# Kernel tuning notes

Hardware: AMD Instinct MI355X
Metric: run time of the kernel (lower is better)

## Reference

```python
import jax, jax.numpy as jnp
import numpy as np


def setup_inputs() -> dict:
    key = jax.random.key(0)
    ks = jax.random.split(key, 7)
    B, IN, H = 4096, 2048, 2048
    initrange = 1.0 / np.sqrt(H)
    return {
        "x": jax.random.normal(ks[0], (B, IN), dtype=jnp.float32),
        "h_prev": jax.random.normal(ks[1], (B, H), dtype=jnp.float32),
        "c_prev": jax.random.normal(ks[2], (B, H), dtype=jnp.float32),
        "W_x": jax.random.uniform(ks[3], (4 * H, IN), minval=-initrange, maxval=initrange, dtype=jnp.float32),
        "b_x": jax.random.uniform(ks[4], (4 * H,), minval=-initrange, maxval=initrange, dtype=jnp.float32),
        "W_h": jax.random.uniform(ks[5], (4 * H, H), minval=-initrange, maxval=initrange, dtype=jnp.float32),
        "b_h": jax.random.uniform(ks[6], (4 * H,), minval=-initrange, maxval=initrange, dtype=jnp.float32),
    }


def reference(x, h_prev, c_prev, W_x, b_x, W_h, b_h):
    # gates = Linear_x(x) + Linear_h(h_prev), shape [B, 4H]
    gates = x @ W_x.T + b_x + h_prev @ W_h.T + b_h
    i, f, g, o = jnp.split(gates, 4, axis=1)  # chunk order in original: i, f, g, o
    i = jax.nn.sigmoid(i)
    f = jax.nn.sigmoid(f)
    g = jnp.tanh(g)
    o = jax.nn.sigmoid(o)
    c = f * c_prev + i * g
    h = o * jnp.tanh(c)
    return (h, c)
```

## Files before the change

### kernel.cpp

```cpp
#include <hip/hip_runtime.h>
#include <hip/hip_bf16.h>
#include <stdint.h>


#define M_DIM 4096
#define N_PACK 8192
#define K_DIM 4096
#define H_DIM 2048

typedef __attribute__((ext_vector_type(8))) short bf16x8;
typedef __attribute__((ext_vector_type(4))) float f32x4;
typedef __attribute__((ext_vector_type(8))) unsigned short ushortx8;

__device__ __forceinline__ unsigned short f2bf(float f) {
    union { float f; uint32_t u; } v; v.f = f;
    uint32_t u = v.u;
    uint32_t r = (u + 0x7FFFu + ((u >> 16) & 1u)) >> 16;
    return (unsigned short)r;
}

__device__ __forceinline__ float fsigmoid(float x) { return 1.0f / (1.0f + __expf(-x)); }
__device__ __forceinline__ float ftanh(float x) { return 2.0f * fsigmoid(2.0f * x) - 1.0f; }

__global__ __launch_bounds__(256) void pack_a(const float* __restrict__ x,
                                              const float* __restrict__ h,
                                              unsigned short* __restrict__ A) {
    int i = blockIdx.x * 256 + threadIdx.x;
    int e = i * 8;
    int row = e >> 12;
    int col = e & 4095;
    const float* src = (col < H_DIM) ? (x + (size_t)row * H_DIM + col)
                                     : (h + (size_t)row * H_DIM + (col - H_DIM));
    float4 f0 = ((const float4*)src)[0];
    float4 f1 = ((const float4*)src)[1];
    ushortx8 o;
    o[0] = f2bf(f0.x); o[1] = f2bf(f0.y); o[2] = f2bf(f0.z); o[3] = f2bf(f0.w);
    o[4] = f2bf(f1.x); o[5] = f2bf(f1.y); o[6] = f2bf(f1.z); o[7] = f2bf(f1.w);
    *(ushortx8*)(A + e) = o;
}

__global__ __launch_bounds__(256) void pack_w(const float* __restrict__ Wx,
                                              const float* __restrict__ Wh,
                                              unsigned short* __restrict__ W) {
    int i = blockIdx.x * 256 + threadIdx.x;
    int e = i * 8;
    int p = e >> 12;
    int k = e & 4095;
    int g  = (p >> 4) & 3;
    int j  = ((p >> 6) << 4) | (p & 15);
    int orig = g * H_DIM + j;
    const float* src = (k < H_DIM) ? (Wx + (size_t)orig * H_DIM + k)
                                   : (Wh + (size_t)orig * H_DIM + (k - H_DIM));
    float4 f0 = ((const float4*)src)[0];
    float4 f1 = ((const float4*)src)[1];
    ushortx8 o;
    o[0] = f2bf(f0.x); o[1] = f2bf(f0.y); o[2] = f2bf(f0.z); o[3] = f2bf(f0.w);
    o[4] = f2bf(f1.x); o[5] = f2bf(f1.y); o[6] = f2bf(f1.z); o[7] = f2bf(f1.w);
    *(ushortx8*)(W + (size_t)p * K_DIM + k) = o;
}

__device__ __forceinline__ void gload_lds16(const void* g, void* l) {
    __builtin_amdgcn_global_load_lds(
        (const __attribute__((address_space(1))) void*)g,
        (__attribute__((address_space(3))) void*)l, 16, 0, 0);
}

__global__ __launch_bounds__(256, 2) void lstm_gemm(
        const unsigned short* __restrict__ A,
        const unsigned short* __restrict__ W,
        const float* __restrict__ bx, const float* __restrict__ bh,
        const float* __restrict__ c_prev, float* __restrict__ out) {
    __shared__ unsigned short Asm[128 * 64];
    __shared__ unsigned short Bsm[128 * 64];

    const int tid  = threadIdx.x;
    const int wid  = tid >> 6;
    const int lane = tid & 63;
    const int bid  = blockIdx.x;
    const int bm   = bid & 31;
    const int bn   = bid >> 5;
    const int wr   = wid >> 1;
    const int wc   = wid & 1;

    f32x4 acc[4][4] = {};

    const char* Abase = (const char*)A + (size_t)(bm * 128) * (K_DIM * 2);
    const char* Wbase = (const char*)W + (size_t)(bn * 128) * (K_DIM * 2);

    int srow[4], skbs[4];
    #pragma unroll
    for (int q = 0; q < 4; ++q) {
        int chunk = wid * 4 + q;
        int o = chunk * 1024 + lane * 16;
        int row = o >> 7;
        int kb  = o & 127;
        srow[q] = row;
        skbs[q] = kb ^ ((row & 7) << 4);
    }

    for (int kt = 0; kt < K_DIM / 64; ++kt) {
        #pragma unroll
        for (int q = 0; q < 4; ++q) {
            int chunk = wid * 4 + q;
            const char* ga = Abase + (size_t)srow[q] * (K_DIM * 2) + kt * 128 + skbs[q];
            const char* gb = Wbase + (size_t)srow[q] * (K_DIM * 2) + kt * 128 + skbs[q];
            gload_lds16(ga, (char*)Asm + chunk * 1024);
            gload_lds16(gb, (char*)Bsm + chunk * 1024);
        }
        __syncthreads();

        #pragma unroll
        for (int kk = 0; kk < 2; ++kk) {
            bf16x8 af[4], bfr[4];
            #pragma unroll
            for (int m = 0; m < 4; ++m) {
                int row = wr * 64 + m * 16 + (lane & 15);
                int cb  = (kk * 64 + ((lane >> 4) << 4)) ^ ((row & 7) << 4);
                af[m] = *(const bf16x8*)((const char*)Asm + row * 128 + cb);
            }
            #pragma unroll
            for (int n = 0; n < 4; ++n) {
                int row = wc * 64 + n * 16 + (lane & 15);
                int cb  = (kk * 64 + ((lane >> 4) << 4)) ^ ((row & 7) << 4);
                bfr[n] = *(const bf16x8*)((const char*)Bsm + row * 128 + cb);
            }
            #pragma unroll
            for (int m = 0; m < 4; ++m)
                #pragma unroll
                for (int n = 0; n < 4; ++n)
                    acc[m][n] = __builtin_amdgcn_mfma_f32_16x16x32_bf16(
                        af[m], bfr[n], acc[m][n], 0, 0, 0);
        }
        __syncthreads();
    }

    const int jlo  = lane & 15;
    const int rgrp = lane >> 4;
    const int pb   = bn * 128 + wc * 64;
    const int j    = ((pb >> 6) << 4) + jlo;

    const float bi  = bx[j]             + bh[j];
    const float bff = bx[H_DIM + j]     + bh[H_DIM + j];
    const float bg  = bx[2 * H_DIM + j] + bh[2 * H_DIM + j];
    const float bo  = bx[3 * H_DIM + j] + bh[3 * H_DIM + j];

    float* out_h = out;
    float* out_c = out + (size_t)M_DIM * H_DIM;

    #pragma unroll
    for (int m = 0; m < 4; ++m) {
        int row0 = bm * 128 + wr * 64 + m * 16 + rgrp * 4;
        #pragma unroll
        for (int r = 0; r < 4; ++r) {
            int row = row0 + r;
            float pi = acc[m][0][r] + bi;
            float pf = acc[m][1][r] + bff;
            float pg = acc[m][2][r] + bg;
            float po = acc[m][3][r] + bo;
            float i_ = fsigmoid(pi);
            float f_ = fsigmoid(pf);
            float g_ = ftanh(pg);
            float o_ = fsigmoid(po);
            float cp = c_prev[(size_t)row * H_DIM + j];
            float c  = f_ * cp + i_ * g_;
            float hh = o_ * ftanh(c);
            out_h[(size_t)row * H_DIM + j] = hh;
            out_c[(size_t)row * H_DIM + j] = c;
        }
    }
}

extern "C" void kernel_launch(void* const* d_in, const int* in_sizes, int n_in,
                              void* d_out, int out_size, void* d_ws, size_t ws_size,
                              hipStream_t stream) {
    const float* x      = (const float*)d_in[0];
    const float* h_prev = (const float*)d_in[1];
    const float* c_prev = (const float*)d_in[2];
    const float* Wx     = (const float*)d_in[3];
    const float* bx     = (const float*)d_in[4];
    const float* Wh     = (const float*)d_in[5];
    const float* bh     = (const float*)d_in[6];

    unsigned short* Acat = (unsigned short*)d_ws;
    unsigned short* Wp   = (unsigned short*)d_ws + (size_t)M_DIM * K_DIM;

    float* out = (float*)d_out;

    pack_a<<<8192, 256, 0, stream>>>(x, h_prev, Acat);
    pack_w<<<16384, 256, 0, stream>>>(Wx, Wh, Wp);
    lstm_gemm<<<2048, 256, 0, stream>>>(Acat, Wp, bx, bh, c_prev, out);
}
```

Baseline: 492.8 us.

## Rewrite GEMM as 256x256 tile, 8-wave, double-buffered pipelined kernel

Replaces the 128x128 single-buffered GEMM with a 256x256 tile computed by 8 waves. LDS is double-buffered and global-to-LDS loads are staged in quarter-tile pieces interleaved with MFMA phases, using explicit vmcnt/lgkmcnt waits and s_setprio. The block index is swizzled for L2 locality, and each operand load now feeds more MFMAs. The cost is many barriers per k-step, higher register pressure from 32 accumulators per lane, and 128KB of LDS per block, which limits occupancy to one block per CU.

```diff
diff --git a/kernel.cpp b/kernel.cpp
--- a/kernel.cpp
+++ b/kernel.cpp
@@ -65,79 +65,135 @@
         (__attribute__((address_space(3))) void*)l, 16, 0, 0);
 }
 
-__global__ __launch_bounds__(256, 2) void lstm_gemm(
+#define BAR() __builtin_amdgcn_s_barrier()
+#define LGKM0() asm volatile("s_waitcnt lgkmcnt(0)" ::: "memory")
+#define VMCNT2() asm volatile("s_waitcnt vmcnt(2)" ::: "memory")
+#define VMCNT0() asm volatile("s_waitcnt vmcnt(0)" ::: "memory")
+
+__global__ __launch_bounds__(512, 2) void lstm_gemm8(
         const unsigned short* __restrict__ A,
         const unsigned short* __restrict__ W,
         const float* __restrict__ bx, const float* __restrict__ bh,
         const float* __restrict__ c_prev, float* __restrict__ out) {
-    __shared__ unsigned short Asm[128 * 64];
-    __shared__ unsigned short Bsm[128 * 64];
+    __shared__ char lds[2][2][32768];
 
     const int tid  = threadIdx.x;
     const int wid  = tid >> 6;
     const int lane = tid & 63;
-    const int bid  = blockIdx.x;
-    const int bm   = bid & 31;
-    const int bn   = bid >> 5;
-    const int wr   = wid >> 1;
-    const int wc   = wid & 1;
-
-    f32x4 acc[4][4] = {};
-
-    const char* Abase = (const char*)A + (size_t)(bm * 128) * (K_DIM * 2);
-    const char* Wbase = (const char*)W + (size_t)(bn * 128) * (K_DIM * 2);
-
-    int srow[4], skbs[4];
-    #pragma unroll
-    for (int q = 0; q < 4; ++q) {
-        int chunk = wid * 4 + q;
-        int o = chunk * 1024 + lane * 16;
-        int row = o >> 7;
-        int kb  = o & 127;
-        srow[q] = row;
-        skbs[q] = kb ^ ((row & 7) << 4);
-    }
-
-    for (int kt = 0; kt < K_DIM / 64; ++kt) {
-        #pragma unroll
-        for (int q = 0; q < 4; ++q) {
-            int chunk = wid * 4 + q;
-            const char* ga = Abase + (size_t)srow[q] * (K_DIM * 2) + kt * 128 + skbs[q];
-            const char* gb = Wbase + (size_t)srow[q] * (K_DIM * 2) + kt * 128 + skbs[q];
-            gload_lds16(ga, (char*)Asm + chunk * 1024);
-            gload_lds16(gb, (char*)Bsm + chunk * 1024);
-        }
-        __syncthreads();
-
-        #pragma unroll
-        for (int kk = 0; kk < 2; ++kk) {
-            bf16x8 af[4], bfr[4];
+    const int wr   = wid >> 2;
+    const int wc   = wid & 3;
+
+    const int swz = (blockIdx.x & 7) * 64 + (blockIdx.x >> 3);
+    const int bm  = swz & 15;
+    const int bn  = swz >> 4;
+
+    const char* Ab = (const char*)A + (size_t)(bm * 256) * (K_DIM * 2);
+    const char* Wb = (const char*)W + (size_t)(bn * 256) * (K_DIM * 2);
+
+    const int srow = tid >> 3;
+    const int skb  = ((tid & 7) << 4) ^ ((srow & 7) << 4);
+
+    auto stage_half = [&](int buf, int mat, int h, int kt) {
+        const char* gb = mat ? Wb : Ab;
+        #pragma unroll
+        for (int qq = 0; qq < 2; ++qq) {
+            int q = h * 2 + qq;
+            const char* src = gb + (size_t)(q * 64 + srow) * (K_DIM * 2) + kt * 128 + skb;
+            gload_lds16(src, &lds[buf][mat][q * 8192 + tid * 16]);
+        }
+    };
+
+    f32x4 acc[8][4] = {};
+    bf16x8 A0[4][2], A1[4][2], Bq[2][2];
+
+    auto read_a = [&](int buf, int qm, bf16x8 (&ar)[4][2]) {
+        #pragma unroll
+        for (int mf = 0; mf < 4; ++mf) {
+            int row = wr * 128 + (qm * 4 + mf) * 16 + (lane & 15);
             #pragma unroll
-            for (int m = 0; m < 4; ++m) {
-                int row = wr * 64 + m * 16 + (lane & 15);
-                int cb  = (kk * 64 + ((lane >> 4) << 4)) ^ ((row & 7) << 4);
-                af[m] = *(const bf16x8*)((const char*)Asm + row * 128 + cb);
+            for (int kk = 0; kk < 2; ++kk) {
+                int cb = (kk * 64 + ((lane >> 4) << 4)) ^ ((row & 7) << 4);
+                ar[mf][kk] = *(const bf16x8*)&lds[buf][0][row * 128 + cb];
             }
+        }
+    };
+    auto read_b = [&](int buf, int qn) {
+        #pragma unroll
+        for (int nf = 0; nf < 2; ++nf) {
+            int row = wc * 64 + (qn * 2 + nf) * 16 + (lane & 15);
             #pragma unroll
-            for (int n = 0; n < 4; ++n) {
-                int row = wc * 64 + n * 16 + (lane & 15);
-                int cb  = (kk * 64 + ((lane >> 4) << 4)) ^ ((row & 7) << 4);
-                bfr[n] = *(const bf16x8*)((const char*)Bsm + row * 128 + cb);
+            for (int kk = 0; kk < 2; ++kk) {
+                int cb = (kk * 64 + ((lane >> 4) << 4)) ^ ((row & 7) << 4);
+                Bq[nf][kk] = *(const bf16x8*)&lds[buf][1][row * 128 + cb];
             }
-            #pragma unroll
-            for (int m = 0; m < 4; ++m)
-                #pragma unroll
-                for (int n = 0; n < 4; ++n)
-                    acc[m][n] = __builtin_amdgcn_mfma_f32_16x16x32_bf16(
-                        af[m], bfr[n], acc[m][n], 0, 0, 0);
-        }
-        __syncthreads();
+        }
+    };
+
+#define MMA_Q(QM, QN, AR)                                                      \
+    do {                                                                       \
+        __builtin_amdgcn_s_setprio(1);                                         \
+        _Pragma("unroll")                                                      \
+        for (int mf = 0; mf < 4; ++mf) {                                       \
+            _Pragma("unroll")                                                  \
+            for (int nf = 0; nf < 2; ++nf) {                                   \
+                _Pragma("unroll")                                              \
+                for (int kk = 0; kk < 2; ++kk) {                               \
+                    acc[(QM)*4+mf][(QN)*2+nf] =                                \
+                        __builtin_amdgcn_mfma_f32_16x16x32_bf16(               \
+                            AR[mf][kk], Bq[nf][kk],                            \
+                            acc[(QM)*4+mf][(QN)*2+nf], 0, 0, 0);               \
+                }                                                              \
+            }                                                                  \
+        }                                                                      \
+        __builtin_amdgcn_s_setprio(0);                                         \
+    } while (0)
+
+    stage_half(0, 0, 0, 0); stage_half(0, 0, 1, 0);
+    stage_half(0, 1, 0, 0); stage_half(0, 1, 1, 0);
+    stage_half(1, 0, 0, 1);
+    VMCNT2();
+    BAR();
+
+    for (int it = 0; it < 32; ++it) {
+        const int t1   = 2 * it + 1;
+        const bool last = (it == 31);
+
+        read_a(0, 0, A0); read_b(0, 0);
+        stage_half(1, 0, 1, t1);
+        BAR(); LGKM0(); MMA_Q(0, 0, A0); BAR();
+
+        read_a(0, 1, A1);
+        stage_half(1, 1, 0, t1);
+        BAR(); LGKM0(); MMA_Q(1, 0, A1); BAR();
+
+        read_b(0, 1);
+        stage_half(1, 1, 1, t1);
+        BAR(); LGKM0(); MMA_Q(0, 1, A0); BAR();
+
+        if (!last) { stage_half(0, 0, 0, t1 + 1); VMCNT2(); }
+        else       { VMCNT0(); }
+        BAR(); LGKM0(); MMA_Q(1, 1, A1); BAR();
+
+        read_a(1, 0, A0); read_b(1, 0);
+        if (!last) stage_half(0, 0, 1, t1 + 1);
+        BAR(); LGKM0(); MMA_Q(0, 0, A0); BAR();
+
+        read_a(1, 1, A1);
+        if (!last) stage_half(0, 1, 0, t1 + 1);
+        BAR(); LGKM0(); MMA_Q(1, 0, A1); BAR();
+
+        read_b(1, 1);
+        if (!last) stage_half(0, 1, 1, t1 + 1);
+        BAR(); LGKM0(); MMA_Q(0, 1, A0); BAR();
+
+        if (!last) { stage_half(1, 0, 0, t1 + 2); VMCNT2(); }
+        else       { VMCNT0(); }
+        BAR(); LGKM0(); MMA_Q(1, 1, A1); BAR();
     }
 
     const int jlo  = lane & 15;
     const int rgrp = lane >> 4;
-    const int pb   = bn * 128 + wc * 64;
-    const int j    = ((pb >> 6) << 4) + jlo;
+    const int j    = (bn * 4 + wc) * 16 + jlo;
 
     const float bi  = bx[j]             + bh[j];
     const float bff = bx[H_DIM + j]     + bh[H_DIM + j];
@@ -148,8 +204,8 @@
     float* out_c = out + (size_t)M_DIM * H_DIM;
 
     #pragma unroll
-    for (int m = 0; m < 4; ++m) {
-        int row0 = bm * 128 + wr * 64 + m * 16 + rgrp * 4;
+    for (int m = 0; m < 8; ++m) {
+        int row0 = bm * 256 + wr * 128 + m * 16 + rgrp * 4;
         #pragma unroll
         for (int r = 0; r < 4; ++r) {
             int row = row0 + r;
@@ -188,5 +244,5 @@
 
     pack_a<<<8192, 256, 0, stream>>>(x, h_prev, Acat);
     pack_w<<<16384, 256, 0, stream>>>(Wx, Wh, Wp);
-    lstm_gemm<<<2048, 256, 0, stream>>>(Acat, Wp, bx, bh, c_prev, out);
-}
+    lstm_gemm8<<<512, 512, 0, stream>>>(Acat, Wp, bx, bh, c_prev, out);
+}
```

After: 474.8 us. 3.7% less time.
